# Optimization experiments

Measured on AMD Instinct MI355X. Metric: run time of the kernel, lower is better.

The kernel has to match this reference:

```python
import jax, jax.numpy as jnp
import numpy as np

IN_SHAPE = (192, 192, 192)
N_CH = 1
BATCH = 2
VOLUME_RES = np.array([1.0, 1.0, 1.0], dtype=np.float32)
MIN_SUB_RES = np.array([1.0, 1.0, 1.0], dtype=np.float32)
RESAMPLE_SHAPE = (192, 192, 192)
# shape of the intermediate (downsampled-then-stored) grid, as in build():
DOWN_GRID_SHAPE = tuple(int(s) for s in np.int32(np.array(IN_SHAPE) * VOLUME_RES / MIN_SUB_RES))


def _ndgrid(shape):
    # [*shape, ndims] float32 coordinate grid (tf ndgrid equivalent)
    return jnp.stack(jnp.meshgrid(*[jnp.arange(s, dtype=jnp.float32) for s in shape], indexing='ij'), axis=-1)


def _interp_nearest(vol, loc):
    # vol: [X,Y,Z,C], loc: [...,3] -> gather at rounded, clipped coords
    max_loc = jnp.asarray([vol.shape[d] - 1 for d in range(3)], dtype=jnp.float32)
    idx = jnp.clip(jnp.round(loc), 0.0, max_loc).astype(jnp.int32)
    return vol[idx[..., 0], idx[..., 1], idx[..., 2]]


def _interp_linear(vol, loc):
    # faithful port of neurite interpn(..., 'linear'): 8-corner gather + weighted sum
    max_loc = [float(vol.shape[d] - 1) for d in range(3)]
    loc = jnp.stack([jnp.clip(loc[..., d], 0.0, max_loc[d]) for d in range(3)], axis=-1)
    loc0 = jnp.floor(loc)
    f0 = jnp.stack([jnp.clip(loc0[..., d], 0.0, max_loc[d]) for d in range(3)], axis=-1)
    f1 = jnp.stack([jnp.clip(loc0[..., d] + 1.0, 0.0, max_loc[d]) for d in range(3)], axis=-1)
    w0 = f1 - loc          # weight for floor corner (diff_loc1 in neurite)
    w1 = 1.0 - w0          # weight for ceil corner
    i0 = f0.astype(jnp.int32)
    i1 = f1.astype(jnp.int32)
    out = jnp.zeros(loc.shape[:-1] + (vol.shape[-1],), dtype=vol.dtype)
    for c in range(8):  # fixed 2^ndims corner loop
        bits = [(c >> d) & 1 for d in range(3)]
        idx = tuple((i1 if b else i0)[..., d] for d, b in enumerate(bits))
        w = jnp.ones(loc.shape[:-1], dtype=vol.dtype)
        for d, b in enumerate(bits):
            w = w * (w1 if b else w0)[..., d]
        out = out + w[..., None] * vol[idx]
    return out


def setup_inputs() -> dict:
    key = jax.random.key(0)
    k1, k2 = jax.random.split(key)
    vol = jax.random.normal(k1, (BATCH, *IN_SHAPE, N_CH), dtype=jnp.float32)
    # subsample resolutions must be >= min_subsample_res (=1.0)
    subsample_res = jax.random.uniform(k2, (BATCH, 3), dtype=jnp.float32, minval=1.0, maxval=4.0)
    return {"vol": vol, "subsample_res": subsample_res}


def reference(vol, subsample_res):
    inshape_f = jnp.asarray(IN_SHAPE, dtype=jnp.float32)
    # down_shape = int32(inshape * volume_res / subsample_res)  per example, [B,3]
    down_shape = (inshape_f * jnp.asarray(VOLUME_RES) / subsample_res).astype(jnp.int32)
    down_zoom = down_shape.astype(jnp.float32) / inshape_f                               # [B,3]
    up_zoom = jnp.asarray(RESAMPLE_SHAPE, dtype=jnp.float32) / down_shape.astype(jnp.float32)  # [B,3]
    down_grid = _ndgrid(DOWN_GRID_SHAPE)    # [X,Y,Z,3]
    up_grid = _ndgrid(RESAMPLE_SHAPE)       # [X',Y',Z',3]

    def one(v, dz, uz):
        # pass 1: nearest resample at acquisition resolution (clip to [0, inshape] as in layer)
        down_loc = jnp.clip(down_grid / dz, 0.0, inshape_f)
        mid = _interp_nearest(v, down_loc)
        # pass 2: trilinear resample back to resample_shape
        up_loc = up_grid / uz
        return _interp_linear(mid, up_loc)

    return jax.vmap(one)(vol, down_zoom, up_zoom)
```

## Files before the change

kernel.cpp:

```cpp
#include <hip/hip_runtime.h>
#include <hip/hip_fp16.h>

#define DIM 192
#define RMAX 26

typedef float v2f __attribute__((ext_vector_type(2)));

__device__ __forceinline__ int nearest_map(int t, float dz) {
    float dl = (float)t / dz;
    dl = fminf(fmaxf(dl, 0.0f), 192.0f);
    float r = rintf(dl);
    r = fminf(r, 191.0f);
    return (int)r;
}

__device__ __forceinline__ void lut_entry(int i, float uz, float dz,
                                          float& w0, int& n0, int& n1) {
    float l = (float)i / uz;
    l = fminf(fmaxf(l, 0.0f), 191.0f);
    const float f0 = floorf(l);
    const float f1 = fminf(f0 + 1.0f, 191.0f);
    w0 = f1 - l;
    n0 = nearest_map((int)f0, dz);
    n1 = nearest_map((int)f1, dz);
}

__device__ __forceinline__ unsigned int pack_h2(float a, float b) {
    __half2 h = __floats2half2_rn(a, b);
    return *reinterpret_cast<unsigned int*>(&h);
}

__device__ __forceinline__ v2f unpack_h2(unsigned int u) {
    __half2 h = *reinterpret_cast<__half2*>(&u);
    float2 f = __half22float2(h);
    v2f r; r.x = f.x; r.y = f.y;
    return r;
}

__global__ __launch_bounds__(256, 8) void mimic_acq_one_kernel(
    const float* __restrict__ vol,
    const float* __restrict__ sres,
    float* __restrict__ out)
{
    __shared__ unsigned int lds[RMAX * DIM];
    __shared__ float yw[16];
    __shared__ int   yn0[16], yn1[16];

    const int tz  = threadIdx.x;
    const int ty  = threadIdx.y;
    const int tid = ty * 64 + tz;

    const int bid = blockIdx.x;
    const int wg  = (bid & 7) * 576 + (bid >> 3);
    const int bx  = wg / 12;
    const int tile = wg % 12;
    const int b   = (bx >= DIM) ? 1 : 0;
    const int x   = bx - b * DIM;
    const int y0t = tile * 16;

    const float srx = sres[b * 3 + 0];
    const float sry = sres[b * 3 + 1];
    const float srz = sres[b * 3 + 2];
    const float dsxf = (float)(int)(192.0f / srx);
    const float dsyf = (float)(int)(192.0f / sry);
    const float dszf = (float)(int)(192.0f / srz);
    const float uzx = 192.0f / dsxf, dzx = dsxf / 192.0f;
    const float uzy = 192.0f / dsyf, dzy = dsyf / 192.0f;
    const float uzz = 192.0f / dszf, dzz = dszf / 192.0f;

    float w0x; int nx0, nx1;
    lut_entry(x, uzx, dzx, w0x, nx0, nx1);
    const float w1x = 1.0f - w0x;

    float wt_; int nymin, nt_, nb_, nymax;
    lut_entry(y0t,      uzy, dzy, wt_, nymin, nt_);
    lut_entry(y0t + 15, uzy, dzy, wt_, nb_,   nymax);
    const int R = nymax - nymin + 1;

    if (tid < 16) {
        float w0; int n0, n1;
        lut_entry(y0t + tid, uzy, dzy, w0, n0, n1);
        yw[tid]  = w0;
        yn0[tid] = n0;
        yn1[tid] = n1;
    }

    {
        const float* vb = vol + (size_t)b * (DIM * DIM * DIM);
        const float* r0 = vb + ((size_t)nx0 * DIM + nymin) * DIM;
        const float* r1 = vb + ((size_t)nx1 * DIM + nymin) * DIM;
        const int C = R * 48;
        for (int c = tid; c < C; c += 256) {
            const int yy = c / 48;
            const int z4 = (c - yy * 48) * 4;
            const float4 v0 = *(const float4*)(r0 + yy * DIM + z4);
            const float4 v1 = *(const float4*)(r1 + yy * DIM + z4);
            uint4 q;
            q.x = pack_h2(v0.x, v1.x);
            q.y = pack_h2(v0.y, v1.y);
            q.z = pack_h2(v0.z, v1.z);
            q.w = pack_h2(v0.w, v1.w);
            *(uint4*)&lds[yy * DIM + z4] = q;
        }
    }

    float w0zk[3];
    int   zz0[3], zz1[3];
#pragma unroll
    for (int k = 0; k < 3; ++k) {
        lut_entry(tz + k * 64, uzz, dzz, w0zk[k], zz0[k], zz1[k]);
    }

    __syncthreads();

#pragma unroll
    for (int yj = 0; yj < 4; ++yj) {
        const int ly = ty * 4 + yj;
        const int y  = y0t + ly;
        const float w0y = yw[ly], w1y = 1.0f - w0y;
        const int rr0 = (yn0[ly] - nymin) * DIM;
        const int rr1 = (yn1[ly] - nymin) * DIM;
        float* ob = out + ((size_t)bx * DIM + y) * DIM + tz;
#pragma unroll
        for (int k = 0; k < 3; ++k) {
            const v2f p00 = unpack_h2(lds[rr0 + zz0[k]]);
            const v2f p01 = unpack_h2(lds[rr1 + zz0[k]]);
            const v2f p10 = unpack_h2(lds[rr0 + zz1[k]]);
            const v2f p11 = unpack_h2(lds[rr1 + zz1[k]]);
            const float wz0 = w0zk[k];
            const float wz1 = 1.0f - wz0;
            const v2f l0 = p00 * wz0 + p10 * wz1;
            const v2f l1 = p01 * wz0 + p11 * wz1;
            const v2f m  = l0 * w0y + l1 * w1y;
            const float r = m.x * w0x + m.y * w1x;
            __builtin_nontemporal_store(r, ob + k * 64);
        }
    }
}

extern "C" void kernel_launch(void* const* d_in, const int* in_sizes, int n_in,
                              void* d_out, int out_size, void* d_ws, size_t ws_size,
                              hipStream_t stream) {
    const float* vol  = (const float*)d_in[0];
    const float* sres = (const float*)d_in[1];
    float* out = (float*)d_out;

    dim3 block(64, 4, 1);
    dim3 grid(4608, 1, 1);
    hipLaunchKernelGGL(mimic_acq_one_kernel, grid, block, 0, stream, vol, sres, out);
}
```

Baseline: 30.14 us.

## Compute z/y lerp in packed fp16 and build LUTs cooperatively in shared memory

Moves the z and y interpolation math from fp32 (after unpacking half2) to packed fp16 vector ops, which removes the conversions and halves the ALU work. The per-thread LUT computation, with its divisions, is replaced by a cooperative build into shared memory: one entry per thread for z, 16 for y, and one for x, packed as a half weight plus two 8-bit indices, followed by an extra barrier. The trade is fp16 weight and accumulation error, an added __syncthreads, and an LDS row count reduced from 26 to 25, which could overflow if the row span exceeds that bound.

Result: faster. 24.29 us, median of 2 (-19.4%).

```diff
diff --git a/kernel.cpp b/kernel.cpp
--- a/kernel.cpp
+++ b/kernel.cpp
@@ -2,9 +2,9 @@
 #include <hip/hip_fp16.h>
 
 #define DIM 192
-#define RMAX 26
+#define RROWS 25
 
-typedef float v2f __attribute__((ext_vector_type(2)));
+typedef _Float16 h2v __attribute__((ext_vector_type(2)));
 
 __device__ __forceinline__ int nearest_map(int t, float dz) {
     float dl = (float)t / dz;
@@ -14,15 +14,19 @@
     return (int)r;
 }
 
-__device__ __forceinline__ void lut_entry(int i, float uz, float dz,
-                                          float& w0, int& n0, int& n1) {
+__device__ __forceinline__ unsigned int make_entry(int i, float sr) {
+    const float dsf = (float)(int)(192.0f / sr);
+    const float uz  = 192.0f / dsf;
+    const float dz  = dsf / 192.0f;
     float l = (float)i / uz;
     l = fminf(fmaxf(l, 0.0f), 191.0f);
     const float f0 = floorf(l);
     const float f1 = fminf(f0 + 1.0f, 191.0f);
-    w0 = f1 - l;
-    n0 = nearest_map((int)f0, dz);
-    n1 = nearest_map((int)f1, dz);
+    const float w0 = f1 - l;
+    const int n0 = nearest_map((int)f0, dz);
+    const int n1 = nearest_map((int)f1, dz);
+    const __half hw = __float2half(w0);
+    return (unsigned int)__half_as_ushort(hw) | ((unsigned int)n0 << 16) | ((unsigned int)n1 << 24);
 }
 
 __device__ __forceinline__ unsigned int pack_h2(float a, float b) {
@@ -30,21 +34,28 @@
     return *reinterpret_cast<unsigned int*>(&h);
 }
 
-__device__ __forceinline__ v2f unpack_h2(unsigned int u) {
-    __half2 h = *reinterpret_cast<__half2*>(&u);
-    float2 f = __half22float2(h);
-    v2f r; r.x = f.x; r.y = f.y;
-    return r;
+__device__ __forceinline__ h2v as_h2v(unsigned int u) {
+    union { unsigned int u; h2v h; } cv;
+    cv.u = u;
+    return cv.h;
 }
 
-__global__ __launch_bounds__(256, 8) void mimic_acq_one_kernel(
+__device__ __forceinline__ h2v bcast_h(unsigned int u) {
+    union { unsigned int u; h2v h; } cv;
+    cv.u = (u & 0xffffu) * 0x10001u;
+    return cv.h;
+}
+
+__global__ __launch_bounds__(256, 8) void mimic_acq_f1_kernel(
     const float* __restrict__ vol,
     const float* __restrict__ sres,
     float* __restrict__ out)
 {
-    __shared__ unsigned int lds[RMAX * DIM];
-    __shared__ float yw[16];
-    __shared__ int   yn0[16], yn1[16];
+    __shared__ unsigned int lds[RROWS * DIM];
+    __shared__ unsigned int zside[DIM];
+    __shared__ unsigned int yside[16];
+    __shared__ float xw_s;
+    __shared__ unsigned int xn_s;
 
     const int tz  = threadIdx.x;
     const int ty  = threadIdx.y;
@@ -58,32 +69,31 @@
     const int x   = bx - b * DIM;
     const int y0t = tile * 16;
 
-    const float srx = sres[b * 3 + 0];
-    const float sry = sres[b * 3 + 1];
-    const float srz = sres[b * 3 + 2];
-    const float dsxf = (float)(int)(192.0f / srx);
-    const float dsyf = (float)(int)(192.0f / sry);
-    const float dszf = (float)(int)(192.0f / srz);
-    const float uzx = 192.0f / dsxf, dzx = dsxf / 192.0f;
-    const float uzy = 192.0f / dsyf, dzy = dsyf / 192.0f;
-    const float uzz = 192.0f / dszf, dzz = dszf / 192.0f;
+    if (tid < DIM) {
+        zside[tid] = make_entry(tid, sres[b * 3 + 2]);
+    } else if (tid < DIM + 16) {
+        yside[tid - DIM] = make_entry(y0t + (tid - DIM), sres[b * 3 + 1]);
+    } else if (tid == DIM + 16) {
+        const float srx = sres[b * 3 + 0];
+        const float dsf = (float)(int)(192.0f / srx);
+        const float uz  = 192.0f / dsf;
+        const float dz  = dsf / 192.0f;
+        float l = (float)x / uz;
+        l = fminf(fmaxf(l, 0.0f), 191.0f);
+        const float f0 = floorf(l);
+        const float f1 = fminf(f0 + 1.0f, 191.0f);
+        xw_s = f1 - l;
+        xn_s = (unsigned int)nearest_map((int)f0, dz)
+             | ((unsigned int)nearest_map((int)f1, dz) << 8);
+    }
+    __syncthreads();
 
-    float w0x; int nx0, nx1;
-    lut_entry(x, uzx, dzx, w0x, nx0, nx1);
-    const float w1x = 1.0f - w0x;
-
-    float wt_; int nymin, nt_, nb_, nymax;
-    lut_entry(y0t,      uzy, dzy, wt_, nymin, nt_);
-    lut_entry(y0t + 15, uzy, dzy, wt_, nb_,   nymax);
-    const int R = nymax - nymin + 1;
-
-    if (tid < 16) {
-        float w0; int n0, n1;
-        lut_entry(y0t + tid, uzy, dzy, w0, n0, n1);
-        yw[tid]  = w0;
-        yn0[tid] = n0;
-        yn1[tid] = n1;
-    }
+    const float w0x = xw_s, w1x = 1.0f - xw_s;
+    const unsigned int xpk = xn_s;
+    const int nx0 = (int)(xpk & 0xffu);
+    const int nx1 = (int)(xpk >> 8);
+    const int nymin = (int)((yside[0] >> 16) & 0xffu);
+    const int R = (int)(yside[15] >> 24) - nymin + 1;
 
     {
         const float* vb = vol + (size_t)b * (DIM * DIM * DIM);
@@ -104,11 +114,16 @@
         }
     }
 
-    float w0zk[3];
-    int   zz0[3], zz1[3];
+    h2v wz0h[3], wz1h[3];
+    int zz0[3], zz1[3];
+    const h2v ones = { (_Float16)1.0f, (_Float16)1.0f };
 #pragma unroll
     for (int k = 0; k < 3; ++k) {
-        lut_entry(tz + k * 64, uzz, dzz, w0zk[k], zz0[k], zz1[k]);
+        const unsigned int u = zside[tz + k * 64];
+        wz0h[k] = bcast_h(u);
+        wz1h[k] = ones - wz0h[k];
+        zz0[k]  = (int)((u >> 16) & 0xffu);
+        zz1[k]  = (int)(u >> 24);
     }
 
     __syncthreads();
@@ -117,22 +132,24 @@
     for (int yj = 0; yj < 4; ++yj) {
         const int ly = ty * 4 + yj;
         const int y  = y0t + ly;
-        const float w0y = yw[ly], w1y = 1.0f - w0y;
-        const int rr0 = (yn0[ly] - nymin) * DIM;
-        const int rr1 = (yn1[ly] - nymin) * DIM;
+        const unsigned int uy = yside[ly];
+        const h2v w0yh = bcast_h(uy);
+        const h2v w1yh = ones - w0yh;
+        const int rr0 = ((int)((uy >> 16) & 0xffu) - nymin) * DIM;
+        const int rr1 = ((int)(uy >> 24) - nymin) * DIM;
         float* ob = out + ((size_t)bx * DIM + y) * DIM + tz;
 #pragma unroll
         for (int k = 0; k < 3; ++k) {
-            const v2f p00 = unpack_h2(lds[rr0 + zz0[k]]);
-            const v2f p01 = unpack_h2(lds[rr1 + zz0[k]]);
-            const v2f p10 = unpack_h2(lds[rr0 + zz1[k]]);
-            const v2f p11 = unpack_h2(lds[rr1 + zz1[k]]);
-            const float wz0 = w0zk[k];
-            const float wz1 = 1.0f - wz0;
-            const v2f l0 = p00 * wz0 + p10 * wz1;
-            const v2f l1 = p01 * wz0 + p11 * wz1;
-            const v2f m  = l0 * w0y + l1 * w1y;
-            const float r = m.x * w0x + m.y * w1x;
+            const h2v p00 = as_h2v(lds[rr0 + zz0[k]]);
+            const h2v p01 = as_h2v(lds[rr1 + zz0[k]]);
+            const h2v p10 = as_h2v(lds[rr0 + zz1[k]]);
+            const h2v p11 = as_h2v(lds[rr1 + zz1[k]]);
+
+            const h2v l0 = p00 * wz0h[k] + p10 * wz1h[k];
+            const h2v l1 = p01 * wz0h[k] + p11 * wz1h[k];
+            const h2v m  = l0 * w0yh + l1 * w1yh;
+
+            const float r = (float)m.x * w0x + (float)m.y * w1x;
             __builtin_nontemporal_store(r, ob + k * 64);
         }
     }
@@ -147,5 +164,5 @@
 
     dim3 block(64, 4, 1);
     dim3 grid(4608, 1, 1);
-    hipLaunchKernelGGL(mimic_acq_one_kernel, grid, block, 0, stream, vol, sres, out);
+    hipLaunchKernelGGL(mimic_acq_f1_kernel, grid, block, 0, stream, vol, sres, out);
 }
```
